# Kernel tuning notes

Measured on AMD Instinct MI355X. Metric: run time of the kernel, lower is better.

Reference implementation:

```python
import jax, jax.numpy as jnp
import numpy as np
import math

B, C, AM, HEADS, F, W = 2, 16, 4, 8, 1024, 1024
HD = F // HEADS


def _conv2d(x, w, b):
    # 3x3 conv, padding=1, NCHW
    y = jax.lax.conv_general_dilated(x, w, (1, 1), ((1, 1), (1, 1)),
                                     dimension_numbers=('NCHW', 'OIHW', 'NCHW'))
    return y + b[None, :, None, None]


def _rotary(x):
    # x: (b, am, heads, w, hd); rotate over seq axis w, interleaved pairs (lucidrains style)
    hd, w = x.shape[-1], x.shape[-2]
    inv = 10000.0 ** (-jnp.arange(0, hd, 2, dtype=jnp.float32) / hd)  # (hd/2,)
    ang = jnp.repeat(jnp.arange(w, dtype=jnp.float32)[:, None] * inv[None, :], 2, axis=-1)  # (w, hd)
    xp = x.reshape(x.shape[:-1] + (hd // 2, 2))
    xr = jnp.stack((-xp[..., 1], xp[..., 0]), axis=-1).reshape(x.shape)
    return x * jnp.cos(ang) + xr * jnp.sin(ang)


def _proj(inp, wc, bc, wpw):
    # conv (c -> am) then per-map linear over feature axis, then split heads
    y = _conv2d(inp, wc, bc)                          # (b, am, F, W)
    y = jnp.einsum('cfh,bchw->bcfw', wpw, y)          # per attention-map linear on features
    b = y.shape[0]
    # transpose(2,3) -> (b, am, W, F) -> (b, am, W, heads, hd) -> (b, am, heads, W, hd)
    return y.transpose(0, 1, 3, 2).reshape(b, AM, W, HEADS, HD).transpose(0, 1, 3, 2, 4)


def _forward(x, prev_qk, mask, wq_conv, bq_conv, wq_pw, wk_conv, bk_conv, wk_pw,
             wv_conv, bv_conv, wv_pw, wo_pw, wo_dw, wo_conv, bo_conv):
    b, c, h, w = x.shape
    q = _rotary(_proj(x, wq_conv, bq_conv, wq_pw))    # (b, am, heads, w, hd)
    k = _rotary(_proj(x, wk_conv, bk_conv, wk_pw))
    v = _proj(x, wv_conv, bv_conv, wv_pw)
    # NOTE: source scales by 1/sqrt(h) where h is the feature (height) dim
    qk = jnp.einsum('bmnqd,bmnkd->bmnqk', q, k) / math.sqrt(h)
    qk = qk + prev_qk + mask                          # additive prev_qk and mask biases
    a = jnp.einsum('bmnqk,bmnkd->bmnqd', jax.nn.softmax(qk, axis=-1), v)
    # merge heads back: (b, am, w, heads*hd) -> (b, am, F, w)
    a = a.transpose(0, 1, 3, 2, 4).reshape(b, AM, w, F).transpose(0, 1, 3, 2)
    # o_linear: depthwise channel mix then per-map feature linear
    a = jnp.einsum('oc,bchw->bohw', wo_dw, a)
    a = jnp.einsum('cfh,bchw->bcfw', wo_pw, a)
    out = _conv2d(jnp.concatenate((x, a), axis=1), wo_conv, bo_conv)
    return out, qk


def setup_inputs() -> dict:
    key = jax.random.key(0)
    ks = jax.random.split(key, 12)
    s = 0.02
    return {
        'x': jax.random.normal(ks[0], (B, C, F, W), jnp.float32),
        'prev_qk': jax.random.normal(ks[1], (B, AM, HEADS, W, W), jnp.float32) * 0.1,
        'mask': jax.random.normal(ks[2], (W, W), jnp.float32) * 0.1,
        'wq_conv': jax.random.normal(ks[3], (AM, C, 3, 3), jnp.float32) * s,
        'bq_conv': jnp.zeros((AM,), jnp.float32),
        'wq_pw': jax.random.normal(ks[4], (AM, F, F), jnp.float32) * s,
        'wk_conv': jax.random.normal(ks[5], (AM, C, 3, 3), jnp.float32) * s,
        'bk_conv': jnp.zeros((AM,), jnp.float32),
        'wk_pw': jax.random.normal(ks[6], (AM, F, F), jnp.float32) * s,
        'wv_conv': jax.random.normal(ks[7], (AM, C, 3, 3), jnp.float32) * s,
        'bv_conv': jnp.zeros((AM,), jnp.float32),
        'wv_pw': jax.random.normal(ks[8], (AM, F, F), jnp.float32) * s,
        'wo_pw': jax.random.normal(ks[9], (AM, F, F), jnp.float32) * s,
        'wo_dw': jax.random.normal(ks[10], (AM, AM), jnp.float32) * 0.2,
        'wo_conv': jax.random.normal(ks[11], (C, C + AM, 3, 3), jnp.float32) * s,
        'bo_conv': jnp.zeros((C,), jnp.float32),
    }


def reference(x, prev_qk, mask, wq_conv, bq_conv, wq_pw, wk_conv, bk_conv, wk_pw,
              wv_conv, bv_conv, wv_pw, wo_pw, wo_dw, wo_conv, bo_conv):
    return _forward(x, prev_qk, mask, wq_conv, bq_conv, wq_pw, wk_conv, bk_conv, wk_pw,
                    wv_conv, bv_conv, wv_pw, wo_pw, wo_dw, wo_conv, bo_conv)
```

## Files before the change

### kernel.cpp

```cpp
#include <hip/hip_runtime.h>


typedef unsigned short u16;
typedef __attribute__((ext_vector_type(8))) short bf16x8;
typedef __attribute__((ext_vector_type(4))) float f32x4;

constexpr size_t EL = 1024ull * 1024ull;

__device__ __forceinline__ u16 f2bf(float f) {
  union { float f; unsigned u; } v; v.f = f;
  return (u16)((v.u + 0x7fffu + ((v.u >> 16) & 1u)) >> 16);
}
__device__ __forceinline__ float bf2f(u16 h) {
  union { unsigned u; float f; } v; v.u = ((unsigned)h) << 16;
  return v.f;
}

__global__ __launch_bounds__(256) void cast_wpw(const float* __restrict__ q,
                                                const float* __restrict__ k,
                                                const float* __restrict__ v,
                                                const float* __restrict__ o,
                                                u16* __restrict__ dst) {
  size_t i = (size_t)blockIdx.x * 256 + threadIdx.x;
  int mat = (int)(i >> 22);
  size_t off = i & 4194303ull;
  const float* s = (mat == 0) ? q : (mat == 1) ? k : (mat == 2) ? v : o;
  dst[i] = f2bf(s[off]);
}

__global__ __launch_bounds__(256) void conv_qkv(
    const float* __restrict__ x, const float* __restrict__ wq,
    const float* __restrict__ bq, const float* __restrict__ wk,
    const float* __restrict__ bk, const float* __restrict__ wv,
    const float* __restrict__ bv, u16* __restrict__ yTq,
    u16* __restrict__ yTk, u16* __restrict__ yTv) {
  __shared__ float xt[18 * 18];
  const int b = blockIdx.z;
  const int f0 = blockIdx.y * 16, w0 = blockIdx.x * 16;
  const int tx = threadIdx.x & 15;
  const int ty = threadIdx.x >> 4;
  float acc[12];
#pragma unroll
  for (int p = 0; p < 12; ++p) acc[p] = 0.f;
  for (int c = 0; c < 16; ++c) {
    __syncthreads();
    const float* xc = x + ((size_t)(b * 16 + c) << 20);
    for (int idx = threadIdx.x; idx < 324; idx += 256) {
      int r = idx / 18, cc = idx - r * 18;
      int gf = f0 - 1 + r, gw = w0 - 1 + cc;
      float val = 0.f;
      if ((unsigned)gf < 1024u && (unsigned)gw < 1024u)
        val = xc[((size_t)gf << 10) + gw];
      xt[idx] = val;
    }
    __syncthreads();
    float xv[9];
#pragma unroll
    for (int ky = 0; ky < 3; ++ky)
#pragma unroll
      for (int kx = 0; kx < 3; ++kx)
        xv[ky * 3 + kx] = xt[(tx + ky) * 18 + (ty + kx)];
#pragma unroll
    for (int m = 0; m < 4; ++m) {
      const float* wqc = wq + (m * 16 + c) * 9;
      const float* wkc = wk + (m * 16 + c) * 9;
      const float* wvc = wv + (m * 16 + c) * 9;
#pragma unroll
      for (int t = 0; t < 9; ++t) {
        acc[m]     += xv[t] * wqc[t];
        acc[4 + m] += xv[t] * wkc[t];
        acc[8 + m] += xv[t] * wvc[t];
      }
    }
  }
  const int w = w0 + ty, f = f0 + tx;
#pragma unroll
  for (int m = 0; m < 4; ++m) {
    size_t o = ((((size_t)(b * 4 + m) << 10) + w) << 10) + f;
    yTq[o] = f2bf(acc[m] + bq[m]);
    yTk[o] = f2bf(acc[4 + m] + bk[m]);
    yTv[o] = f2bf(acc[8 + m] + bv[m]);
  }
}

template <int MODE>
__global__ __launch_bounds__(256) void gemm_pw(const u16* __restrict__ Aall,
                                               const u16* __restrict__ Ball,
                                               u16* __restrict__ Call) {
  const int z = blockIdx.z;
  const int am = z & 3;
  const u16* __restrict__ A = Aall + (size_t)am * EL;
  const u16* __restrict__ Bt = Ball + (size_t)z * EL;
  const int bm = blockIdx.y * 128;
  const int bn = blockIdx.x * 128;
  __shared__ u16 As[128 * 40];
  __shared__ u16 Bs[128 * 40];
  const int tid = threadIdx.x;
  const int lane = tid & 63, wv = tid >> 6;
  const int wm = (wv >> 1) * 64, wn = (wv & 1) * 64;
  const int mrow = lane & 15, quad = lane >> 4;
  const f32x4 fz = {0.f, 0.f, 0.f, 0.f};
  f32x4 acc[4][4];
#pragma unroll
  for (int i = 0; i < 4; ++i)
#pragma unroll
    for (int j = 0; j < 4; ++j) acc[i][j] = fz;

  for (int k0 = 0; k0 < 1024; k0 += 32) {
#pragma unroll
    for (int i = 0; i < 2; ++i) {
      const int cc = tid + i * 256;
      const int row = cc >> 2;
      const int kb = (cc & 3) * 8;
      *(uint4*)(As + row * 40 + kb) =
          *(const uint4*)(A + (size_t)(bm + row) * 1024 + (k0 + kb));
      *(uint4*)(Bs + row * 40 + kb) =
          *(const uint4*)(Bt + (size_t)(bn + row) * 1024 + (k0 + kb));
    }
    __syncthreads();
    bf16x8 af[4], bfv[4];
#pragma unroll
    for (int t = 0; t < 4; ++t) {
      af[t]  = *(const bf16x8*)(As + (wm + 16 * t + mrow) * 40 + quad * 8);
      bfv[t] = *(const bf16x8*)(Bs + (wn + 16 * t + mrow) * 40 + quad * 8);
    }
#pragma unroll
    for (int mt = 0; mt < 4; ++mt)
#pragma unroll
      for (int nt = 0; nt < 4; ++nt)
        acc[mt][nt] = __builtin_amdgcn_mfma_f32_16x16x32_bf16(
            af[mt], bfv[nt], acc[mt][nt], 0, 0, 0);
    __syncthreads();
  }

  if (MODE == 0) {
    u16* C = Call + (size_t)z * EL;
#pragma unroll
    for (int mt = 0; mt < 4; ++mt) {
      const int rowb = bm + wm + 16 * mt + quad * 4;
#pragma unroll
      for (int nt = 0; nt < 4; ++nt) {
        const int col = bn + wn + 16 * nt + mrow;
#pragma unroll
        for (int r = 0; r < 4; ++r)
          C[(size_t)(rowb + r) * 1024 + col] = f2bf(acc[mt][nt][r]);
      }
    }
  } else {
    u16* C = Call + (size_t)z * EL;
    const int head = blockIdx.y;
#pragma unroll
    for (int mt = 0; mt < 4; ++mt) {
      const int d0 = wm + 16 * mt + quad * 4;
      const float i1 = (float)(d0 >> 1);
      const float inv1 = __powf(10000.f, -i1 * (1.f / 64.f));
      const float inv2 = __powf(10000.f, -(i1 + 1.f) * (1.f / 64.f));
#pragma unroll
      for (int nt = 0; nt < 4; ++nt) {
        const int w = bn + wn + 16 * nt + mrow;
        float s1, c1, s2, c2;
        __sincosf((float)w * inv1, &s1, &c1);
        __sincosf((float)w * inv2, &s2, &c2);
        const float x0 = acc[mt][nt][0], x1 = acc[mt][nt][1];
        const float x2 = acc[mt][nt][2], x3 = acc[mt][nt][3];
        ushort4 o4;
        o4.x = f2bf(x0 * c1 - x1 * s1);
        o4.y = f2bf(x1 * c1 + x0 * s1);
        o4.z = f2bf(x2 * c2 - x3 * s2);
        o4.w = f2bf(x3 * c2 + x2 * s2);
        *(ushort4*)(C + ((size_t)head * 1024 + w) * 128 + d0) = o4;
      }
    }
  }
}

__global__ __launch_bounds__(256) void gemm_s(const u16* __restrict__ Qt,
                                              const u16* __restrict__ Kt,
                                              const float* __restrict__ prev,
                                              const float* __restrict__ mask,
                                              float* __restrict__ Sout) {
  const int z = blockIdx.z;
  const u16* __restrict__ A = Qt + (size_t)z * (EL / 8);
  const u16* __restrict__ Bt = Kt + (size_t)z * (EL / 8);
  const int bm = blockIdx.y * 128;
  const int bn = blockIdx.x * 128;
  __shared__ u16 As[128 * 40];
  __shared__ u16 Bs[128 * 40];
  const int tid = threadIdx.x;
  const int lane = tid & 63, wv = tid >> 6;
  const int wm = (wv >> 1) * 64, wn = (wv & 1) * 64;
  const int mrow = lane & 15, quad = lane >> 4;
  const f32x4 fz = {0.f, 0.f, 0.f, 0.f};
  f32x4 acc[4][4];
#pragma unroll
  for (int i = 0; i < 4; ++i)
#pragma unroll
    for (int j = 0; j < 4; ++j) acc[i][j] = fz;

  for (int k0 = 0; k0 < 128; k0 += 32) {
#pragma unroll
    for (int i = 0; i < 2; ++i) {
      const int cc = tid + i * 256;
      const int row = cc >> 2;
      const int kb = (cc & 3) * 8;
      *(uint4*)(As + row * 40 + kb) =
          *(const uint4*)(A + (size_t)(bm + row) * 128 + (k0 + kb));
      *(uint4*)(Bs + row * 40 + kb) =
          *(const uint4*)(Bt + (size_t)(bn + row) * 128 + (k0 + kb));
    }
    __syncthreads();
    bf16x8 af[4], bfv[4];
#pragma unroll
    for (int t = 0; t < 4; ++t) {
      af[t]  = *(const bf16x8*)(As + (wm + 16 * t + mrow) * 40 + quad * 8);
      bfv[t] = *(const bf16x8*)(Bs + (wn + 16 * t + mrow) * 40 + quad * 8);
    }
#pragma unroll
    for (int mt = 0; mt < 4; ++mt)
#pragma unroll
      for (int nt = 0; nt < 4; ++nt)
        acc[mt][nt] = __builtin_amdgcn_mfma_f32_16x16x32_bf16(
            af[mt], bfv[nt], acc[mt][nt], 0, 0, 0);
    __syncthreads();
  }
  const float* P = prev + (size_t)z * EL;
  float* S = Sout + (size_t)z * EL;
#pragma unroll
  for (int mt = 0; mt < 4; ++mt) {
    const int rowb = bm + wm + 16 * mt + quad * 4;
#pragma unroll
    for (int nt = 0; nt < 4; ++nt) {
      const int col = bn + wn + 16 * nt + mrow;
#pragma unroll
      for (int r = 0; r < 4; ++r) {
        const size_t idx = (size_t)(rowb + r) * 1024 + col;
        S[idx] = acc[mt][nt][r] * 0.03125f + P[idx] + mask[idx];
      }
    }
  }
}

__global__ __launch_bounds__(256) void softmax_stats(
    const float* __restrict__ S, float* __restrict__ rmax,
    float* __restrict__ rsinv) {
  const size_t row = blockIdx.x;
  const float* r = S + row * 1024;
  const int t = threadIdx.x;
  float4 v = *(const float4*)(r + t * 4);
  float m = fmaxf(fmaxf(v.x, v.y), fmaxf(v.z, v.w));
  __shared__ float red[256];
  red[t] = m;
  __syncthreads();
  for (int s = 128; s > 0; s >>= 1) {
    if (t < s) red[t] = fmaxf(red[t], red[t + s]);
    __syncthreads();
  }
  const float gm = red[0];
  __syncthreads();
  float e = __expf(v.x - gm) + __expf(v.y - gm) + __expf(v.z - gm) +
            __expf(v.w - gm);
  red[t] = e;
  __syncthreads();
  for (int s = 128; s > 0; s >>= 1) {
    if (t < s) red[t] += red[t + s];
    __syncthreads();
  }
  if (t == 0) {
    rmax[row] = gm;
    rsinv[row] = 1.f / red[0];
  }
}

__global__ __launch_bounds__(256) void gemm_pv(const float* __restrict__ Sfull,
                                               const u16* __restrict__ Vn,
                                               const float* __restrict__ rmax,
                                               const float* __restrict__ rsinv,
                                               u16* __restrict__ AT) {
  const int z = blockIdx.z;
  const int bam = z >> 3, head = z & 7;
  const float* __restrict__ A = Sfull + (size_t)z * EL;
  const u16* __restrict__ Bt =
      Vn + (size_t)bam * EL + (size_t)head * 128 * 1024;
  const int bm = blockIdx.y * 128;
  __shared__ float Asf[128 * 36];
  __shared__ u16 Bs[128 * 40];
  __shared__ float smax[128], ssinv[128];
  const int tid = threadIdx.x;
  if (tid < 128) {
    smax[tid] = rmax[(size_t)z * 1024 + bm + tid];
    ssinv[tid] = rsinv[(size_t)z * 1024 + bm + tid];
  }
  const int lane = tid & 63, wv = tid >> 6;
  const int wm = (wv >> 1) * 64, wn = (wv & 1) * 64;
  const int mrow = lane & 15, quad = lane >> 4;
  const f32x4 fz = {0.f, 0.f, 0.f, 0.f};
  f32x4 acc[4][4];
#pragma unroll
  for (int i = 0; i < 4; ++i)
#pragma unroll
    for (int j = 0; j < 4; ++j) acc[i][j] = fz;

  for (int k0 = 0; k0 < 1024; k0 += 32) {
#pragma unroll
    for (int i = 0; i < 4; ++i) {
      const int cc = tid + i * 256;
      const int row = cc >> 3;
      const int kf = (cc & 7) * 4;
      *(float4*)(Asf + row * 36 + kf) =
          *(const float4*)(A + (size_t)(bm + row) * 1024 + (k0 + kf));
    }
#pragma unroll
    for (int i = 0; i < 2; ++i) {
      const int cc = tid + i * 256;
      const int row = cc >> 2;
      const int kb = (cc & 3) * 8;
      *(uint4*)(Bs + row * 40 + kb) =
          *(const uint4*)(Bt + (size_t)row * 1024 + (k0 + kb));
    }
    __syncthreads();
    bf16x8 af[4], bfv[4];
#pragma unroll
    for (int t = 0; t < 4; ++t) {
      const int m = wm + 16 * t + mrow;
      const float* ap = Asf + m * 36 + quad * 8;
      const float mx = smax[m], si = ssinv[m];
      bf16x8 av;
#pragma unroll
      for (int j = 0; j < 8; ++j) {
        const float p = __expf(ap[j] - mx) * si;
        av[j] = (short)f2bf(p);
      }
      af[t] = av;
      bfv[t] = *(const bf16x8*)(Bs + (wn + 16 * t + mrow) * 40 + quad * 8);
    }
#pragma unroll
    for (int mt = 0; mt < 4; ++mt)
#pragma unroll
      for (int nt = 0; nt < 4; ++nt)
        acc[mt][nt] = __builtin_amdgcn_mfma_f32_16x16x32_bf16(
            af[mt], bfv[nt], acc[mt][nt], 0, 0, 0);
    __syncthreads();
  }
  u16* C = AT + (size_t)bam * EL + (size_t)head * 128;
#pragma unroll
  for (int mt = 0; mt < 4; ++mt) {
    const int rowb = bm + wm + 16 * mt + quad * 4;
#pragma unroll
    for (int nt = 0; nt < 4; ++nt) {
      const int col = wn + 16 * nt + mrow;
#pragma unroll
      for (int r = 0; r < 4; ++r)
        C[(size_t)(rowb + r) * 1024 + col] = f2bf(acc[mt][nt][r]);
    }
  }
}

__global__ __launch_bounds__(256) void mix_dw(const u16* __restrict__ AT,
                                              const float* __restrict__ dw,
                                              u16* __restrict__ a2T) {
  const size_t i = (size_t)blockIdx.x * 256 + threadIdx.x;
  const int b = (int)(i >> 18);
  const size_t pos = (i & 262143ull) << 2;
  const u16* bb = AT + (size_t)b * 4 * EL + pos;
  float4 v[4];
#pragma unroll
  for (int c = 0; c < 4; ++c) {
    ushort4 t = *(const ushort4*)(bb + (size_t)c * EL);
    v[c].x = bf2f(t.x); v[c].y = bf2f(t.y); v[c].z = bf2f(t.z); v[c].w = bf2f(t.w);
  }
#pragma unroll
  for (int o = 0; o < 4; ++o) {
    const float w0 = dw[o * 4 + 0], w1 = dw[o * 4 + 1];
    const float w2 = dw[o * 4 + 2], w3 = dw[o * 4 + 3];
    ushort4 s;
    s.x = f2bf(w0 * v[0].x + w1 * v[1].x + w2 * v[2].x + w3 * v[3].x);
    s.y = f2bf(w0 * v[0].y + w1 * v[1].y + w2 * v[2].y + w3 * v[3].y);
    s.z = f2bf(w0 * v[0].z + w1 * v[1].z + w2 * v[2].z + w3 * v[3].z);
    s.w = f2bf(w0 * v[0].w + w1 * v[1].w + w2 * v[2].w + w3 * v[3].w);
    *(ushort4*)(a2T + (size_t)b * 4 * EL + (size_t)o * EL + pos) = s;
  }
}

__global__ __launch_bounds__(256) void conv_out(const float* __restrict__ x,
                                                const u16* __restrict__ a3,
                                                const float* __restrict__ wo,
                                                const float* __restrict__ bo,
                                                float* __restrict__ out) {
  __shared__ float xt[18 * 18];
  const int b = blockIdx.z;
  const int f0 = blockIdx.y * 16, w0 = blockIdx.x * 16;
  const int tx = threadIdx.x & 15;
  const int ty = threadIdx.x >> 4;
  float acc[16];
#pragma unroll
  for (int o = 0; o < 16; ++o) acc[o] = bo[o];
  for (int c = 0; c < 20; ++c) {
    __syncthreads();
    for (int idx = threadIdx.x; idx < 324; idx += 256) {
      int r = idx / 18, cc = idx - r * 18;
      int gf = f0 - 1 + r, gw = w0 - 1 + cc;
      float val = 0.f;
      if ((unsigned)gf < 1024u && (unsigned)gw < 1024u) {
        if (c < 16)
          val = x[(((size_t)(b * 16 + c) << 10) + gf) * 1024 + gw];
        else
          val = bf2f(a3[(((size_t)(b * 4 + (c - 16)) << 10) + gf) * 1024 + gw]);
      }
      xt[idx] = val;
    }
    __syncthreads();
    float xv[9];
#pragma unroll
    for (int ky = 0; ky < 3; ++ky)
#pragma unroll
      for (int kx = 0; kx < 3; ++kx)
        xv[ky * 3 + kx] = xt[(ty + ky) * 18 + (tx + kx)];
#pragma unroll
    for (int o = 0; o < 16; ++o) {
      const float* wc = wo + (o * 20 + c) * 9;
#pragma unroll
      for (int t = 0; t < 9; ++t) acc[o] += xv[t] * wc[t];
    }
  }
  const int f = f0 + ty, w = w0 + tx;
#pragma unroll
  for (int o = 0; o < 16; ++o)
    out[(((size_t)(b * 16 + o) << 10) + f) * 1024 + w] = acc[o];
}

extern "C" void kernel_launch(void* const* d_in, const int* in_sizes, int n_in,
                              void* d_out, int out_size, void* d_ws,
                              size_t ws_size, hipStream_t stream) {
  const float* x       = (const float*)d_in[0];
  const float* prev_qk = (const float*)d_in[1];
  const float* mask    = (const float*)d_in[2];
  const float* wq_conv = (const float*)d_in[3];
  const float* bq_conv = (const float*)d_in[4];
  const float* wq_pw   = (const float*)d_in[5];
  const float* wk_conv = (const float*)d_in[6];
  const float* bk_conv = (const float*)d_in[7];
  const float* wk_pw   = (const float*)d_in[8];
  const float* wv_conv = (const float*)d_in[9];
  const float* bv_conv = (const float*)d_in[10];
  const float* wv_pw   = (const float*)d_in[11];
  const float* wo_pw   = (const float*)d_in[12];
  const float* wo_dw   = (const float*)d_in[13];
  const float* wo_conv = (const float*)d_in[14];
  const float* bo_conv = (const float*)d_in[15];

  float* out = (float*)d_out;
  float* qk  = out + 32 * EL;

  u16* ws16 = (u16*)d_ws;
  u16* wpwQ = ws16;
  u16* wpwK = ws16 + 4 * EL;
  u16* wpwV = ws16 + 8 * EL;
  u16* wpwO = ws16 + 12 * EL;
  u16* yTq  = ws16 + 16 * EL;
  u16* yTk  = yTq + 8 * EL;
  u16* yTv  = yTk + 8 * EL;
  u16* Qt   = yTv + 8 * EL;
  u16* Kt   = Qt + 8 * EL;
  u16* Vn   = Kt + 8 * EL;
  u16* AT   = Vn + 8 * EL;
  u16* a2T  = AT + 8 * EL;
  u16* a3   = a2T + 8 * EL;
  float* rmax  = (float*)(a3 + 8 * EL);
  float* rsinv = rmax + 65536;

  cast_wpw<<<65536, 256, 0, stream>>>(wq_pw, wk_pw, wv_pw, wo_pw, ws16);
  conv_qkv<<<dim3(64, 64, 2), 256, 0, stream>>>(
      x, wq_conv, bq_conv, wk_conv, bk_conv, wv_conv, bv_conv, yTq, yTk, yTv);
  gemm_pw<1><<<dim3(8, 8, 8), 256, 0, stream>>>(wpwQ, yTq, Qt);
  gemm_pw<1><<<dim3(8, 8, 8), 256, 0, stream>>>(wpwK, yTk, Kt);
  gemm_pw<0><<<dim3(8, 8, 8), 256, 0, stream>>>(wpwV, yTv, Vn);
  gemm_s<<<dim3(8, 8, 64), 256, 0, stream>>>(Qt, Kt, prev_qk, mask, qk);
  softmax_stats<<<65536, 256, 0, stream>>>(qk, rmax, rsinv);
  gemm_pv<<<dim3(1, 8, 64), 256, 0, stream>>>(qk, Vn, rmax, rsinv, AT);
  mix_dw<<<2048, 256, 0, stream>>>(AT, wo_dw, a2T);
  gemm_pw<0><<<dim3(8, 8, 8), 256, 0, stream>>>(wpwO, a2T, a3);
  conv_out<<<dim3(64, 64, 2), 256, 0, stream>>>(x, a3, wo_conv, bo_conv, out);
}
```

Measured before the change: 1.619 ms.

## Fuse QK, softmax and PV into a flash-style online-softmax attention kernel

Replaces the three kernels gemm_s, softmax_stats and gemm_pv with one fused kernel. It computes score tiles, adds prev/mask, writes qk as output, and keeps running max and sum for an online softmax while it accumulates P·V in registers. The goal is to stop re-reading the 256MB fp32 score matrix twice (stats pass and PV pass) and to drop two launches. The cost is a grid of only 512 blocks, each running a serial loop over 16 key tiles with heavy LDS use and several barriers.

```diff
diff --git a/kernel.cpp b/kernel.cpp
--- a/kernel.cpp
+++ b/kernel.cpp
@@ -174,185 +174,184 @@
   }
 }
 
-__global__ __launch_bounds__(256) void gemm_s(const u16* __restrict__ Qt,
-                                              const u16* __restrict__ Kt,
-                                              const float* __restrict__ prev,
-                                              const float* __restrict__ mask,
-                                              float* __restrict__ Sout) {
-  const int z = blockIdx.z;
-  const u16* __restrict__ A = Qt + (size_t)z * (EL / 8);
-  const u16* __restrict__ Bt = Kt + (size_t)z * (EL / 8);
-  const int bm = blockIdx.y * 128;
-  const int bn = blockIdx.x * 128;
-  __shared__ u16 As[128 * 40];
-  __shared__ u16 Bs[128 * 40];
+__global__ __launch_bounds__(256, 2) void attn_fused(
+    const u16* __restrict__ Qt, const u16* __restrict__ Kt,
+    const u16* __restrict__ Vn, const float* __restrict__ prev,
+    const float* __restrict__ maskp, float* __restrict__ Sout,
+    u16* __restrict__ AT) {
+  const int z = blockIdx.y;
+  const int bam = z >> 3, head = z & 7;
+  const int bm = blockIdx.x * 128;
+  const u16* __restrict__ Q = Qt + (size_t)z * (EL / 8);
+  const u16* __restrict__ K = Kt + (size_t)z * (EL / 8);
+  const u16* __restrict__ V =
+      Vn + (size_t)bam * EL + (size_t)head * 128 * 1024;
+  const float* __restrict__ Pz = prev + (size_t)z * EL;
+  float* __restrict__ Sg = Sout + (size_t)z * EL;
+
+  __shared__ __align__(16) char smem[72192];
+  u16* Vs = (u16*)smem;
+  u16* Ps = (u16*)(smem + 18432);
+  float* sfl = (float*)(smem + 36864);
+  float* Sx = (float*)(smem + 37376);
+  u16* Ks = (u16*)(smem + 37376);
+
   const int tid = threadIdx.x;
   const int lane = tid & 63, wv = tid >> 6;
-  const int wm = (wv >> 1) * 64, wn = (wv & 1) * 64;
   const int mrow = lane & 15, quad = lane >> 4;
+  const int wrow = wv * 32;
+  const int prow = lane >> 4;
+  const int pcol4 = (lane & 15) * 4;
+
+  bf16x8 qf[2][4];
+#pragma unroll
+  for (int mt = 0; mt < 2; ++mt)
+#pragma unroll
+    for (int kk = 0; kk < 4; ++kk)
+      qf[mt][kk] = *(const bf16x8*)(
+          Q + (size_t)(bm + wrow + 16 * mt + mrow) * 128 + kk * 32 + quad * 8);
+
   const f32x4 fz = {0.f, 0.f, 0.f, 0.f};
-  f32x4 acc[4][4];
-#pragma unroll
-  for (int i = 0; i < 4; ++i)
-#pragma unroll
-    for (int j = 0; j < 4; ++j) acc[i][j] = fz;
-
-  for (int k0 = 0; k0 < 128; k0 += 32) {
-#pragma unroll
-    for (int i = 0; i < 2; ++i) {
-      const int cc = tid + i * 256;
-      const int row = cc >> 2;
-      const int kb = (cc & 3) * 8;
-      *(uint4*)(As + row * 40 + kb) =
-          *(const uint4*)(A + (size_t)(bm + row) * 128 + (k0 + kb));
-      *(uint4*)(Bs + row * 40 + kb) =
-          *(const uint4*)(Bt + (size_t)(bn + row) * 128 + (k0 + kb));
-    }
-    __syncthreads();
-    bf16x8 af[4], bfv[4];
-#pragma unroll
-    for (int t = 0; t < 4; ++t) {
-      af[t]  = *(const bf16x8*)(As + (wm + 16 * t + mrow) * 40 + quad * 8);
-      bfv[t] = *(const bf16x8*)(Bs + (wn + 16 * t + mrow) * 40 + quad * 8);
-    }
-#pragma unroll
-    for (int mt = 0; mt < 4; ++mt)
+  f32x4 oacc[2][8];
+#pragma unroll
+  for (int mt = 0; mt < 2; ++mt)
+#pragma unroll
+    for (int nt = 0; nt < 8; ++nt) oacc[mt][nt] = fz;
+  float m_st[8], l_st[8];
+#pragma unroll
+  for (int c = 0; c < 8; ++c) { m_st[c] = -3.0e38f; l_st[c] = 0.f; }
+
+  for (int t = 0; t < 16; ++t) {
+    const int kb = t * 64;
+#pragma unroll
+    for (int i = 0; i < 4; ++i) {
+      const int c = tid + i * 256;
+      const int row = c >> 4, c8 = (c & 15) * 8;
+      *(uint4*)(Ks + row * 136 + c8) =
+          *(const uint4*)(K + (size_t)(kb + row) * 128 + c8);
+    }
+#pragma unroll
+    for (int i = 0; i < 4; ++i) {
+      const int c = tid + i * 256;
+      const int row = c >> 3, c8 = (c & 7) * 8;
+      *(uint4*)(Vs + row * 72 + c8) =
+          *(const uint4*)(V + (size_t)row * 1024 + kb + c8);
+    }
+    __syncthreads();
+
+    f32x4 sacc[2][4];
+#pragma unroll
+    for (int mt = 0; mt < 2; ++mt)
+#pragma unroll
+      for (int nt = 0; nt < 4; ++nt) sacc[mt][nt] = fz;
+#pragma unroll
+    for (int kk = 0; kk < 4; ++kk) {
+      bf16x8 bk[4];
 #pragma unroll
       for (int nt = 0; nt < 4; ++nt)
-        acc[mt][nt] = __builtin_amdgcn_mfma_f32_16x16x32_bf16(
-            af[mt], bfv[nt], acc[mt][nt], 0, 0, 0);
-    __syncthreads();
-  }
-  const float* P = prev + (size_t)z * EL;
-  float* S = Sout + (size_t)z * EL;
-#pragma unroll
-  for (int mt = 0; mt < 4; ++mt) {
-    const int rowb = bm + wm + 16 * mt + quad * 4;
-#pragma unroll
-    for (int nt = 0; nt < 4; ++nt) {
-      const int col = bn + wn + 16 * nt + mrow;
+        bk[nt] = *(const bf16x8*)(Ks + (16 * nt + mrow) * 136 + kk * 32 +
+                                  quad * 8);
+#pragma unroll
+      for (int mt = 0; mt < 2; ++mt)
+#pragma unroll
+        for (int nt = 0; nt < 4; ++nt)
+          sacc[mt][nt] = __builtin_amdgcn_mfma_f32_16x16x32_bf16(
+              qf[mt][kk], bk[nt], sacc[mt][nt], 0, 0, 0);
+    }
+    __syncthreads();
+
+#pragma unroll
+    for (int mt = 0; mt < 2; ++mt)
+#pragma unroll
+      for (int nt = 0; nt < 4; ++nt)
+#pragma unroll
+        for (int r = 0; r < 4; ++r)
+          Sx[(wrow + 16 * mt + quad * 4 + r) * 68 + 16 * nt + mrow] =
+              sacc[mt][nt][r];
+
+#pragma unroll
+    for (int c = 0; c < 8; ++c) {
+      const int rloc = wrow + c * 4 + prow;
+      const size_t gidx = (size_t)(bm + rloc) * 1024 + kb + pcol4;
+      f32x4 sx = *(const f32x4*)(Sx + rloc * 68 + pcol4);
+      f32x4 pv = __builtin_nontemporal_load((const f32x4*)(Pz + gidx));
+      f32x4 mv = *(const f32x4*)(maskp + gidx);
+      f32x4 s;
+      s.x = sx.x * 0.03125f + pv.x + mv.x;
+      s.y = sx.y * 0.03125f + pv.y + mv.y;
+      s.z = sx.z * 0.03125f + pv.z + mv.z;
+      s.w = sx.w * 0.03125f + pv.w + mv.w;
+      __builtin_nontemporal_store(s, (f32x4*)(Sg + gidx));
+      float mx = fmaxf(fmaxf(s.x, s.y), fmaxf(s.z, s.w));
+      mx = fmaxf(mx, __shfl_xor(mx, 1, 64));
+      mx = fmaxf(mx, __shfl_xor(mx, 2, 64));
+      mx = fmaxf(mx, __shfl_xor(mx, 4, 64));
+      mx = fmaxf(mx, __shfl_xor(mx, 8, 64));
+      const float mn = fmaxf(m_st[c], mx);
+      const float sf = __expf(m_st[c] - mn);
+      m_st[c] = mn;
+      const float p0 = __expf(s.x - mn), p1 = __expf(s.y - mn);
+      const float p2 = __expf(s.z - mn), p3 = __expf(s.w - mn);
+      float rs = p0 + p1 + p2 + p3;
+      rs += __shfl_xor(rs, 1, 64);
+      rs += __shfl_xor(rs, 2, 64);
+      rs += __shfl_xor(rs, 4, 64);
+      rs += __shfl_xor(rs, 8, 64);
+      l_st[c] = l_st[c] * sf + rs;
+      uint2 pk;
+      pk.x = (unsigned)f2bf(p0) | ((unsigned)f2bf(p1) << 16);
+      pk.y = (unsigned)f2bf(p2) | ((unsigned)f2bf(p3) << 16);
+      *(uint2*)(Ps + rloc * 72 + pcol4) = pk;
+      if ((lane & 15) == 0) sfl[rloc] = sf;
+    }
+
+#pragma unroll
+    for (int mt = 0; mt < 2; ++mt)
 #pragma unroll
       for (int r = 0; r < 4; ++r) {
-        const size_t idx = (size_t)(rowb + r) * 1024 + col;
-        S[idx] = acc[mt][nt][r] * 0.03125f + P[idx] + mask[idx];
+        const float sfv = sfl[wrow + 16 * mt + quad * 4 + r];
+#pragma unroll
+        for (int nt = 0; nt < 8; ++nt) oacc[mt][nt][r] *= sfv;
       }
-    }
-  }
-}
-
-__global__ __launch_bounds__(256) void softmax_stats(
-    const float* __restrict__ S, float* __restrict__ rmax,
-    float* __restrict__ rsinv) {
-  const size_t row = blockIdx.x;
-  const float* r = S + row * 1024;
-  const int t = threadIdx.x;
-  float4 v = *(const float4*)(r + t * 4);
-  float m = fmaxf(fmaxf(v.x, v.y), fmaxf(v.z, v.w));
-  __shared__ float red[256];
-  red[t] = m;
+
+#pragma unroll
+    for (int kk = 0; kk < 2; ++kk) {
+      bf16x8 pa[2], bv[8];
+#pragma unroll
+      for (int mt = 0; mt < 2; ++mt)
+        pa[mt] = *(const bf16x8*)(Ps + (wrow + 16 * mt + mrow) * 72 + kk * 32 +
+                                  quad * 8);
+#pragma unroll
+      for (int nt = 0; nt < 8; ++nt)
+        bv[nt] = *(const bf16x8*)(Vs + (16 * nt + mrow) * 72 + kk * 32 +
+                                  quad * 8);
+#pragma unroll
+      for (int mt = 0; mt < 2; ++mt)
+#pragma unroll
+        for (int nt = 0; nt < 8; ++nt)
+          oacc[mt][nt] = __builtin_amdgcn_mfma_f32_16x16x32_bf16(
+              pa[mt], bv[nt], oacc[mt][nt], 0, 0, 0);
+    }
+    __syncthreads();
+  }
+
+#pragma unroll
+  for (int c = 0; c < 8; ++c)
+    if ((lane & 15) == 0) sfl[wrow + c * 4 + prow] = 1.f / l_st[c];
   __syncthreads();
-  for (int s = 128; s > 0; s >>= 1) {
-    if (t < s) red[t] = fmaxf(red[t], red[t + s]);
-    __syncthreads();
-  }
-  const float gm = red[0];
-  __syncthreads();
-  float e = __expf(v.x - gm) + __expf(v.y - gm) + __expf(v.z - gm) +
-            __expf(v.w - gm);
-  red[t] = e;
-  __syncthreads();
-  for (int s = 128; s > 0; s >>= 1) {
-    if (t < s) red[t] += red[t + s];
-    __syncthreads();
-  }
-  if (t == 0) {
-    rmax[row] = gm;
-    rsinv[row] = 1.f / red[0];
-  }
-}
-
-__global__ __launch_bounds__(256) void gemm_pv(const float* __restrict__ Sfull,
-                                               const u16* __restrict__ Vn,
-                                               const float* __restrict__ rmax,
-                                               const float* __restrict__ rsinv,
-                                               u16* __restrict__ AT) {
-  const int z = blockIdx.z;
-  const int bam = z >> 3, head = z & 7;
-  const float* __restrict__ A = Sfull + (size_t)z * EL;
-  const u16* __restrict__ Bt =
-      Vn + (size_t)bam * EL + (size_t)head * 128 * 1024;
-  const int bm = blockIdx.y * 128;
-  __shared__ float Asf[128 * 36];
-  __shared__ u16 Bs[128 * 40];
-  __shared__ float smax[128], ssinv[128];
-  const int tid = threadIdx.x;
-  if (tid < 128) {
-    smax[tid] = rmax[(size_t)z * 1024 + bm + tid];
-    ssinv[tid] = rsinv[(size_t)z * 1024 + bm + tid];
-  }
-  const int lane = tid & 63, wv = tid >> 6;
-  const int wm = (wv >> 1) * 64, wn = (wv & 1) * 64;
-  const int mrow = lane & 15, quad = lane >> 4;
-  const f32x4 fz = {0.f, 0.f, 0.f, 0.f};
-  f32x4 acc[4][4];
-#pragma unroll
-  for (int i = 0; i < 4; ++i)
-#pragma unroll
-    for (int j = 0; j < 4; ++j) acc[i][j] = fz;
-
-  for (int k0 = 0; k0 < 1024; k0 += 32) {
-#pragma unroll
-    for (int i = 0; i < 4; ++i) {
-      const int cc = tid + i * 256;
-      const int row = cc >> 3;
-      const int kf = (cc & 7) * 4;
-      *(float4*)(Asf + row * 36 + kf) =
-          *(const float4*)(A + (size_t)(bm + row) * 1024 + (k0 + kf));
-    }
-#pragma unroll
-    for (int i = 0; i < 2; ++i) {
-      const int cc = tid + i * 256;
-      const int row = cc >> 2;
-      const int kb = (cc & 3) * 8;
-      *(uint4*)(Bs + row * 40 + kb) =
-          *(const uint4*)(Bt + (size_t)row * 1024 + (k0 + kb));
-    }
-    __syncthreads();
-    bf16x8 af[4], bfv[4];
-#pragma unroll
-    for (int t = 0; t < 4; ++t) {
-      const int m = wm + 16 * t + mrow;
-      const float* ap = Asf + m * 36 + quad * 8;
-      const float mx = smax[m], si = ssinv[m];
-      bf16x8 av;
-#pragma unroll
-      for (int j = 0; j < 8; ++j) {
-        const float p = __expf(ap[j] - mx) * si;
-        av[j] = (short)f2bf(p);
-      }
-      af[t] = av;
-      bfv[t] = *(const bf16x8*)(Bs + (wn + 16 * t + mrow) * 40 + quad * 8);
-    }
-#pragma unroll
-    for (int mt = 0; mt < 4; ++mt)
-#pragma unroll
-      for (int nt = 0; nt < 4; ++nt)
-        acc[mt][nt] = __builtin_amdgcn_mfma_f32_16x16x32_bf16(
-            af[mt], bfv[nt], acc[mt][nt], 0, 0, 0);
-    __syncthreads();
-  }
   u16* C = AT + (size_t)bam * EL + (size_t)head * 128;
 #pragma unroll
-  for (int mt = 0; mt < 4; ++mt) {
-    const int rowb = bm + wm + 16 * mt + quad * 4;
-#pragma unroll
-    for (int nt = 0; nt < 4; ++nt) {
-      const int col = wn + 16 * nt + mrow;
-#pragma unroll
-      for (int r = 0; r < 4; ++r)
-        C[(size_t)(rowb + r) * 1024 + col] = f2bf(acc[mt][nt][r]);
-    }
-  }
+  for (int mt = 0; mt < 2; ++mt)
+#pragma unroll
+    for (int r = 0; r < 4; ++r) {
+      const int rloc = wrow + 16 * mt + quad * 4 + r;
+      const float inv = sfl[rloc];
+      const int grow = bm + rloc;
+#pragma unroll
+      for (int nt = 0; nt < 8; ++nt)
+        C[(size_t)grow * 1024 + 16 * nt + mrow] =
+            f2bf(oacc[mt][nt][r] * inv);
+    }
 }
 
 __global__ __launch_bounds__(256) void mix_dw(const u16* __restrict__ AT,
@@ -465,8 +464,6 @@
   u16* AT   = Vn + 8 * EL;
   u16* a2T  = AT + 8 * EL;
   u16* a3   = a2T + 8 * EL;
-  float* rmax  = (float*)(a3 + 8 * EL);
-  float* rsinv = rmax + 65536;
 
   cast_wpw<<<65536, 256, 0, stream>>>(wq_pw, wk_pw, wv_pw, wo_pw, ws16);
   conv_qkv<<<dim3(64, 64, 2), 256, 0, stream>>>(
@@ -474,9 +471,8 @@
   gemm_pw<1><<<dim3(8, 8, 8), 256, 0, stream>>>(wpwQ, yTq, Qt);
   gemm_pw<1><<<dim3(8, 8, 8), 256, 0, stream>>>(wpwK, yTk, Kt);
   gemm_pw<0><<<dim3(8, 8, 8), 256, 0, stream>>>(wpwV, yTv, Vn);
-  gemm_s<<<dim3(8, 8, 64), 256, 0, stream>>>(Qt, Kt, prev_qk, mask, qk);
-  softmax_stats<<<65536, 256, 0, stream>>>(qk, rmax, rsinv);
-  gemm_pv<<<dim3(1, 8, 64), 256, 0, stream>>>(qk, Vn, rmax, rsinv, AT);
+  attn_fused<<<dim3(8, 64), 256, 0, stream>>>(Qt, Kt, Vn, prev_qk, mask, qk,
+                                              AT);
   mix_dw<<<2048, 256, 0, stream>>>(AT, wo_dw, a2T);
   gemm_pw<0><<<dim3(8, 8, 8), 256, 0, stream>>>(wpwO, a2T, a3);
   conv_out<<<dim3(64, 64, 2), 256, 0, stream>>>(x, a3, wo_conv, bo_conv, out);
```

Measured after the change: 1.384 ms. -14.5%, faster.
